# Kernel optimization log

Hardware: AMD Instinct MI355X
Metric: run time of the kernel (lower is better)

Reference implementation:

```python
import jax, jax.numpy as jnp
import numpy as np
from jax import lax

DN = ('NCHW', 'OIHW', 'NCHW')

def _conv(x, w, b, stride):
    y = lax.conv_general_dilated(x, w, (stride, stride), [(1, 1), (1, 1)], dimension_numbers=DN)
    return y + b[None, :, None, None]

def _deconv(x, w, b):
    # ConvTranspose2d(k=4, stride=2, pad=1) == conv with lhs_dilation=2, pad=k-1-p=2,
    # with w already in flipped OIHW layout.
    y = lax.conv_general_dilated(x, w, (1, 1), [(2, 2), (2, 2)], lhs_dilation=(2, 2), dimension_numbers=DN)
    return y + b[None, :, None, None]

def setup_inputs() -> dict:
    key = jax.random.key(0)
    ks = jax.random.split(key, 14)
    s = 0.05  # keep activations numerically tame
    return {
        'x':   jax.random.normal(ks[0], (16, 3, 256, 256), jnp.float32),
        'ew1': jax.random.normal(ks[1], (64, 3, 4, 4), jnp.float32) * s,
        'eb1': jax.random.normal(ks[2], (64,), jnp.float32) * s,
        'ew2': jax.random.normal(ks[3], (128, 64, 4, 4), jnp.float32) * s,
        'eb2': jax.random.normal(ks[4], (128,), jnp.float32) * s,
        'ew3': jax.random.normal(ks[5], (256, 128, 4, 4), jnp.float32) * s,
        'eb3': jax.random.normal(ks[6], (256,), jnp.float32) * s,
        'cb':  jax.random.normal(ks[7], (8192, 256), jnp.float32),
        'dw1': jax.random.normal(ks[8], (128, 256, 4, 4), jnp.float32) * s,
        'db1': jax.random.normal(ks[9], (128,), jnp.float32) * s,
        'dw2': jax.random.normal(ks[10], (64, 128, 4, 4), jnp.float32) * s,
        'db2': jax.random.normal(ks[11], (64,), jnp.float32) * s,
        'dw3': jax.random.normal(ks[12], (3, 64, 4, 4), jnp.float32) * s,
        'db3': jax.random.normal(ks[13], (3,), jnp.float32) * s,
    }

def reference(x, ew1, eb1, ew2, eb2, ew3, eb3, cb, dw1, db1, dw2, db2, dw3, db3):
    # encoder: 3 stride-2 convs with ReLU between
    h = jax.nn.relu(_conv(x, ew1, eb1, 2))
    h = jax.nn.relu(_conv(h, ew2, eb2, 2))
    feat = _conv(h, ew3, eb3, 2)                     # [B, 256, 32, 32]
    B, C, H, W = feat.shape
    flat = feat.reshape(B, C, H * W).transpose(0, 2, 1)  # [B, HW, C]
    scores = jnp.einsum('btc,kc->btk', flat, cb)     # [B, HW, K] large matrix
    indices = jnp.argmax(scores, axis=-1)            # [B, HW]
    quantized = cb[indices]                          # [B, HW, C]
    q = quantized.transpose(0, 2, 1).reshape(B, C, H, W)
    # decoder: 3 stride-2 transposed convs with ReLU between
    d = jax.nn.relu(_deconv(q, dw1, db1))
    d = jax.nn.relu(_deconv(d, dw2, db2))
    recon = _deconv(d, dw3, db3)                     # [B, 3, 256, 256]
    return recon, indices
```

## Files before the change

kernel.cpp:

```cpp
#include <hip/hip_runtime.h>
#include <hip/hip_fp16.h>
#include <cstdint>
#include <cstddef>

typedef __attribute__((ext_vector_type(8))) short short8;
typedef __attribute__((ext_vector_type(8))) _Float16 h16x8;
typedef __attribute__((ext_vector_type(4))) float f32x4;

__device__ __forceinline__ short f2bf(float x) {
  union { float f; unsigned u; } a; a.f = x;
  unsigned r = a.u + 0x7fff + ((a.u >> 16) & 1);
  return (short)(r >> 16);
}
__device__ __forceinline__ float bf2f(short s) {
  union { unsigned u; float f; } a;
  a.u = ((unsigned)(unsigned short)s) << 16; return a.f;
}
__device__ __forceinline__ void fsplit16(float v, short& h, short& l) {
  __half a = __float2half(v);
  h = (short)__half_as_ushort(a);
  l = (short)__half_as_ushort(__float2half(v - __half2float(a)));
}

__device__ __forceinline__ void ld16(const void* g, void* l) {
  __builtin_amdgcn_global_load_lds(
      (const __attribute__((address_space(1))) unsigned int*)g,
      (__attribute__((address_space(3))) unsigned int*)l, 16, 0, 0);
}

__global__ __launch_bounds__(256) void conv1_kernel(
    const float* __restrict__ x, const float* __restrict__ w,
    const float* __restrict__ bias, short* __restrict__ yh, short* __restrict__ yl)
{
  __shared__ __align__(16) float wl[64 * 48];
  __shared__ float bl[64];
  const int tid = threadIdx.x;
  for (int i = tid; i < 64 * 48; i += 256) wl[i] = w[i];
  if (tid < 64) bl[tid] = bias[tid];
  __syncthreads();
  const int n  = blockIdx.y;
  const int oh = blockIdx.x * 2 + (tid >> 7);
  const int ow = tid & 127;
  const float* xb = x + (size_t)n * 3 * 65536;
  const int ih0 = oh * 2 - 1, iw0 = ow * 2 - 1;
  float xin[48];
#pragma unroll
  for (int ic = 0; ic < 3; ++ic)
#pragma unroll
    for (int kh = 0; kh < 4; ++kh) {
      int ih = ih0 + kh;
      bool rok = (unsigned)ih < 256u;
#pragma unroll
      for (int kw = 0; kw < 4; ++kw) {
        int iw = iw0 + kw;
        xin[ic * 16 + kh * 4 + kw] =
            (rok && (unsigned)iw < 256u) ? xb[ic * 65536 + ih * 256 + iw] : 0.f;
      }
    }
  const size_t ob = ((size_t)n * 16384 + oh * 128 + ow) * 64;
  for (int g = 0; g < 8; ++g) {
    short hs[8], ls[8];
#pragma unroll
    for (int j = 0; j < 8; ++j) {
      const int oc = g * 8 + j;
      float acc = bl[oc];
      const float* wo = &wl[oc * 48];
#pragma unroll
      for (int t = 0; t < 48; ++t) acc = fmaf(wo[t], xin[t], acc);
      acc = fmaxf(acc, 0.f) * 64.f;
      fsplit16(acc, hs[j], ls[j]);
    }
    *(short8*)(yh + ob + g * 8) = *(short8*)hs;
    *(short8*)(yl + ob + g * 8) = *(short8*)ls;
  }
}

template <int COUT, int CIN>
__global__ __launch_bounds__(256) void wpack_conv(
    const float* __restrict__ w, short* __restrict__ Wh, short* __restrict__ Wl)
{
  constexpr int K = 16 * CIN;
  const int idx = blockIdx.x * 256 + threadIdx.x;
  const int oc = idx / K, k = idx - oc * K;
  const int kk = k / CIN, ic = k - kk * CIN;
  const int kh = kk >> 2, kw = kk & 3;
  float v = w[(((size_t)oc * CIN + ic) * 4 + kh) * 4 + kw] * 64.f;
  short h, l;
  fsplit16(v, h, l);
  Wh[idx] = h;
  Wl[idx] = l;
}

template <int CIN, int HIN, int COUTT, bool RELU, bool OUTF>
__global__ __launch_bounds__(256) void conv_mfma(
    const short* __restrict__ inh, const short* __restrict__ inl,
    const short* __restrict__ Wph, const short* __restrict__ Wpl,
    const float* __restrict__ bias,
    short* __restrict__ outh, short* __restrict__ outl,
    float* __restrict__ outf)
{
  constexpr int K = 16 * CIN;
  constexpr int HOUT = HIN / 2;
  constexpr int MT = 128, NPX = 128;
  constexpr int GS = (HOUT == 64) ? 6 : 5;
  constexpr int AE = 4 * MT;
  constexpr int NS = K / 32;
  constexpr float RS = 1.f / 4096.f;
  __shared__ __align__(16) short AhL[2][AE * 8];
  __shared__ __align__(16) short AlL[2][AE * 8];
  __shared__ __align__(16) float bl[MT];
  const int tid = threadIdx.x;
  const int w = tid >> 6, lane = tid & 63;
  const int wm = w >> 1, wn = w & 1;
  const int kgl = lane >> 4, cl = lane & 15;
  const int n = blockIdx.z;
  const int oc0 = blockIdx.y * MT;
  const int oh0 = blockIdx.x * (NPX / HOUT);
  if (tid < MT) bl[tid] = bias[oc0 + tid];

  f32x4 acc[4][4];
#pragma unroll
  for (int i = 0; i < 4; ++i)
#pragma unroll
    for (int j = 0; j < 4; ++j) acc[i][j] = (f32x4){0.f, 0.f, 0.f, 0.f};

  auto stageA = [&](int s, int b) {
    const int kc = s * 32;
#pragma unroll
    for (int rep = 0; rep < AE / 256; ++rep) {
      int e = rep * 256 + tid;
      int kg = e >> 7, oc_l = e & (MT - 1);
      size_t go = (size_t)(oc0 + oc_l) * K + kc + kg * 8;
      int lo = (e & ~63) * 8;
      ld16(Wph + go, &AhL[b][lo]);
      ld16(Wpl + go, &AlL[b][lo]);
    }
  };
  const h16x8 zzh = {0, 0, 0, 0, 0, 0, 0, 0};
  auto loadB = [&](int s, h16x8* bh, h16x8* blv) {
    const int kc = s * 32;
    const int kk = kc / CIN, ic0 = kc % CIN;
    const int kh = kk >> 2, kw = kk & 3;
#pragma unroll
    for (int nt = 0; nt < 4; ++nt) {
      int m = wn * 64 + nt * 16 + cl;
      int ih = 2 * (oh0 + (m >> GS)) - 1 + kh;
      int iw = 2 * (m & (HOUT - 1)) - 1 + kw;
      bool ok = ((unsigned)ih < (unsigned)HIN) && ((unsigned)iw < (unsigned)HIN);
      size_t go = ok ? ((size_t)((n * HIN + ih) * HIN + iw) * CIN + ic0 + kgl * 8)
                     : (size_t)(ic0 + kgl * 8);
      h16x8 vh = *(const h16x8*)(inh + go);
      h16x8 vl = *(const h16x8*)(inl + go);
      bh[nt] = ok ? vh : zzh;
      blv[nt] = ok ? vl : zzh;
    }
  };
  auto compute = [&](int b, const h16x8* bh, const h16x8* blv) {
    h16x8 ah[4], al[4];
#pragma unroll
    for (int mt = 0; mt < 4; ++mt) {
      int row = kgl * MT + wm * 64 + mt * 16 + cl;
      ah[mt] = *(const h16x8*)&AhL[b][row * 8];
      al[mt] = *(const h16x8*)&AlL[b][row * 8];
    }
#pragma unroll
    for (int mt = 0; mt < 4; ++mt)
#pragma unroll
      for (int nt = 0; nt < 4; ++nt) {
        acc[mt][nt] = __builtin_amdgcn_mfma_f32_16x16x32_f16(
            ah[mt], bh[nt], acc[mt][nt], 0, 0, 0);
        acc[mt][nt] = __builtin_amdgcn_mfma_f32_16x16x32_f16(
            ah[mt], blv[nt], acc[mt][nt], 0, 0, 0);
        acc[mt][nt] = __builtin_amdgcn_mfma_f32_16x16x32_f16(
            al[mt], bh[nt], acc[mt][nt], 0, 0, 0);
      }
  };

  h16x8 bhA[4], blA[4], bhB[4], blB[4];
  stageA(0, 0);
  loadB(0, bhA, blA);
  __syncthreads();
  for (int s2 = 0; s2 < NS; s2 += 2) {
    stageA(s2 + 1, 1);
    loadB(s2 + 1, bhB, blB);
    compute(0, bhA, blA);
    __syncthreads();
    if (s2 + 2 < NS) { stageA(s2 + 2, 0); loadB(s2 + 2, bhA, blA); }
    compute(1, bhB, blB);
    __syncthreads();
  }
#pragma unroll
  for (int mt = 0; mt < 4; ++mt) {
    const int oc = wm * 64 + mt * 16 + kgl * 4;
    const float4 bv = *(const float4*)&bl[oc];
#pragma unroll
    for (int nt = 0; nt < 4; ++nt) {
      const int px = wn * 64 + nt * 16 + cl;
      const int oh = oh0 + (px >> GS), ow = px & (HOUT - 1);
      const size_t ob =
          ((size_t)n * (HOUT * HOUT) + oh * HOUT + ow) * COUTT + oc0 + oc;
      float v0 = acc[mt][nt][0] * RS + bv.x;
      float v1 = acc[mt][nt][1] * RS + bv.y;
      float v2 = acc[mt][nt][2] * RS + bv.z;
      float v3 = acc[mt][nt][3] * RS + bv.w;
      if (RELU) {
        v0 = fmaxf(v0, 0.f); v1 = fmaxf(v1, 0.f);
        v2 = fmaxf(v2, 0.f); v3 = fmaxf(v3, 0.f);
      }
      if constexpr (OUTF) {
        ushort4 s;
        s.x = __half_as_ushort(__float2half(v0));
        s.y = __half_as_ushort(__float2half(v1));
        s.z = __half_as_ushort(__float2half(v2));
        s.w = __half_as_ushort(__float2half(v3));
        *(ushort4*)((unsigned short*)outh + ob) = s;
        *(float4*)(outf + ob) = make_float4(v0, v1, v2, v3);
      } else {
        short4 hh, ll;
        fsplit16(v0 * 64.f, hh.x, ll.x);
        fsplit16(v1 * 64.f, hh.y, ll.y);
        fsplit16(v2 * 64.f, hh.z, ll.z);
        fsplit16(v3 * 64.f, hh.w, ll.w);
        *(short4*)(outh + ob) = hh;
        *(short4*)(outl + ob) = ll;
      }
    }
  }
}

__global__ __launch_bounds__(256) void cb_convert(
    const float* __restrict__ cb, short* __restrict__ cbh,
    short* __restrict__ cbl, short* __restrict__ cb16)
{
  const int g = blockIdx.x * 256 + threadIdx.x;
  const float* p = cb + (size_t)g * 8;
  short hs[8], ls[8], fs[8];
#pragma unroll
  for (int u = 0; u < 8; ++u) {
    float v = p[u];
    short h = f2bf(v);
    hs[u] = h;
    ls[u] = f2bf(v - bf2f(h));
    fs[u] = (short)__half_as_ushort(__float2half(v));
  }
  *(short8*)(cbh + (size_t)g * 8) = *(short8*)hs;
  *(short8*)(cbl + (size_t)g * 8) = *(short8*)ls;
  *(short8*)(cb16 + (size_t)g * 8) = *(short8*)fs;
}

__global__ __launch_bounds__(256) void vq_mfma(
    const short* __restrict__ cb16, const short* __restrict__ ft16,
    float4* __restrict__ t4v, int4* __restrict__ t4i)
{
  __shared__ __align__(16) short Ah[2][4 * 128 * 8];
  __shared__ __align__(16) short Bh[2][4 * 128 * 8];
  const int tid = threadIdx.x;
  const int w = tid >> 6, lane = tid & 63;
  const int wm = w >> 1, wn = w & 1;
  const int tok0 = blockIdx.x * 128;
  const int split = blockIdx.y;
  const int kgl = lane >> 4, cl = lane & 15;
  const int i0 = w * 128;

  auto stage = [&](int g, int b) {
    const int tile = g >> 3, s = g & 7;
    const int code0 = split * 1024 + tile * 128;
    const int kc = s * 32;
#pragma unroll
    for (int rep = 0; rep < 2; ++rep) {
      int ib = i0 + rep * 64;
      int i = ib + lane;
      int m = i & 127, kg = i >> 7;
      size_t goffA = (size_t)(code0 + m) * 256 + kc + kg * 8;
      size_t goffB = (size_t)(tok0 + m) * 256 + kc + kg * 8;
      int loff = ib * 8;
      ld16(cb16 + goffA, &Ah[b][loff]);
      ld16(ft16 + goffB, &Bh[b][loff]);
    }
  };

  f32x4 acc[4][4];
  auto compute = [&](bool first, int b) {
    h16x8 ah[4], bh[4];
#pragma unroll
    for (int mt = 0; mt < 4; ++mt) {
      int row = wm * 64 + mt * 16 + cl;
      ah[mt] = *(const h16x8*)&Ah[b][(kgl * 128 + row) * 8];
    }
#pragma unroll
    for (int nt = 0; nt < 4; ++nt) {
      int row = wn * 64 + nt * 16 + cl;
      bh[nt] = *(const h16x8*)&Bh[b][(kgl * 128 + row) * 8];
    }
    if (first) {
#pragma unroll
      for (int mt = 0; mt < 4; ++mt)
#pragma unroll
        for (int nt = 0; nt < 4; ++nt)
          acc[mt][nt] = __builtin_amdgcn_mfma_f32_16x16x32_f16(
              ah[mt], bh[nt], (f32x4){0.f, 0.f, 0.f, 0.f}, 0, 0, 0);
    } else {
#pragma unroll
      for (int mt = 0; mt < 4; ++mt)
#pragma unroll
        for (int nt = 0; nt < 4; ++nt)
          acc[mt][nt] = __builtin_amdgcn_mfma_f32_16x16x32_f16(
              ah[mt], bh[nt], acc[mt][nt], 0, 0, 0);
    }
  };

  float sv1[4], sv2[4];
  int sj1[4], sj2[4];
#pragma unroll
  for (int nt = 0; nt < 4; ++nt) {
    sv1[nt] = -3.4e38f; sv2[nt] = -3.4e38f; sj1[nt] = 0; sj2[nt] = 0;
  }

  stage(0, 0);
  __syncthreads();
  for (int g = 0; g < 64; ++g) {
    if (g + 1 < 64) stage(g + 1, (g + 1) & 1);
    compute((g & 7) == 0, g & 1);
    if ((g & 7) == 7) {
      const int tile = g >> 3;
      const int cb2base = split * 1024 + tile * 128 + wm * 64 + kgl * 4;
#pragma unroll
      for (int nt = 0; nt < 4; ++nt)
#pragma unroll
        for (int mt = 0; mt < 4; ++mt)
#pragma unroll
          for (int r = 0; r < 4; ++r) {
            float v = acc[mt][nt][r];
            int code = cb2base + mt * 16 + r;
            bool g1 = v > sv1[nt];
            bool g2 = v > sv2[nt];
            float nv2 = g1 ? sv1[nt] : (g2 ? v : sv2[nt]);
            int nj2 = g1 ? sj1[nt] : (g2 ? code : sj2[nt]);
            sv1[nt] = g1 ? v : sv1[nt];
            sj1[nt] = g1 ? code : sj1[nt];
            sv2[nt] = nv2; sj2[nt] = nj2;
          }
    }
    __syncthreads();
  }

  float* MrgV = (float*)&Ah[0][0];
  int* MrgI = (int*)&Bh[0][0];
#pragma unroll
  for (int nt = 0; nt < 4; ++nt) {
    float mv[4] = {sv1[nt], sv2[nt], -3.4e38f, -3.4e38f};
    int mj[4] = {sj1[nt], sj2[nt], 0, 0};
#pragma unroll
    for (int st = 16; st < 64; st <<= 1) {
      float ov[4]; int oj[4];
#pragma unroll
      for (int k = 0; k < 4; ++k) {
        ov[k] = __shfl_xor(mv[k], st);
        oj[k] = __shfl_xor(mj[k], st);
      }
#pragma unroll
      for (int k = 0; k < 4; ++k) {
        if (ov[k] > mv[3]) {
          mv[3] = ov[k]; mj[3] = oj[k];
#pragma unroll
          for (int q = 3; q > 0; --q)
            if (mv[q] > mv[q - 1]) {
              float tv = mv[q]; mv[q] = mv[q - 1]; mv[q - 1] = tv;
              int tj = mj[q]; mj[q] = mj[q - 1]; mj[q - 1] = tj;
            }
        }
      }
    }
    if (lane < 16) {
      int tl = wn * 64 + nt * 16 + cl;
#pragma unroll
      for (int k = 0; k < 4; ++k) {
        MrgV[(wm * 128 + tl) * 4 + k] = mv[k];
        MrgI[(wm * 128 + tl) * 4 + k] = mj[k];
      }
    }
  }
  __syncthreads();
  if (tid < 128) {
    int tl = tid;
    float mv[4]; int mj[4];
#pragma unroll
    for (int k = 0; k < 4; ++k) { mv[k] = MrgV[tl * 4 + k]; mj[k] = MrgI[tl * 4 + k]; }
#pragma unroll
    for (int k = 0; k < 4; ++k) {
      float ov = MrgV[(128 + tl) * 4 + k];
      int oj = MrgI[(128 + tl) * 4 + k];
      if (ov > mv[3]) {
        mv[3] = ov; mj[3] = oj;
#pragma unroll
        for (int q = 3; q > 0; --q)
          if (mv[q] > mv[q - 1]) {
            float tv = mv[q]; mv[q] = mv[q - 1]; mv[q - 1] = tv;
            int tj = mj[q]; mj[q] = mj[q - 1]; mj[q - 1] = tj;
          }
      }
    }
    size_t o = (size_t)split * 16384 + tok0 + tl;
    t4v[o] = make_float4(mv[0], mv[1], mv[2], mv[3]);
    t4i[o] = make_int4(mj[0], mj[1], mj[2], mj[3]);
  }
}

__global__ __launch_bounds__(256) void vq_rescore(
    const float4* __restrict__ t4v, const int4* __restrict__ t4i,
    const float* __restrict__ featc, const float* __restrict__ cb,
    int* __restrict__ fidx, float* __restrict__ idx_out)
{
  const int t = blockIdx.x * 256 + threadIdx.x;
  float vs[4] = {-3.4e38f, -3.4e38f, -3.4e38f, -3.4e38f};
  int is[4] = {0, 0, 0, 0};
#pragma unroll
  for (int sp = 0; sp < 8; ++sp) {
    float4 v4 = t4v[(size_t)sp * 16384 + t];
    int4 i4 = t4i[(size_t)sp * 16384 + t];
    float vv[4] = {v4.x, v4.y, v4.z, v4.w};
    int ii[4] = {i4.x, i4.y, i4.z, i4.w};
#pragma unroll
    for (int k = 0; k < 4; ++k) {
      if (vv[k] > vs[3]) {
        vs[3] = vv[k]; is[3] = ii[k];
#pragma unroll
        for (int q = 3; q > 0; --q)
          if (vs[q] > vs[q - 1]) {
            float tv = vs[q]; vs[q] = vs[q - 1]; vs[q - 1] = tv;
            int ti = is[q]; is[q] = is[q - 1]; is[q - 1] = ti;
          }
      }
    }
  }
  const float4* fc = (const float4*)(featc + (size_t)t * 256);
  const float4* c0 = (const float4*)(cb + (size_t)is[0] * 256);
  const float4* c1 = (const float4*)(cb + (size_t)is[1] * 256);
  const float4* c2 = (const float4*)(cb + (size_t)is[2] * 256);
  const float4* c3 = (const float4*)(cb + (size_t)is[3] * 256);
  float s0 = 0.f, s1 = 0.f, s2 = 0.f, s3 = 0.f;
  for (int k4 = 0; k4 < 64; ++k4) {
    float4 f = fc[k4];
    float4 w0 = c0[k4], w1 = c1[k4], w2 = c2[k4], w3 = c3[k4];
    s0 = fmaf(w0.x, f.x, fmaf(w0.y, f.y, fmaf(w0.z, f.z, fmaf(w0.w, f.w, s0))));
    s1 = fmaf(w1.x, f.x, fmaf(w1.y, f.y, fmaf(w1.z, f.z, fmaf(w1.w, f.w, s1))));
    s2 = fmaf(w2.x, f.x, fmaf(w2.y, f.y, fmaf(w2.z, f.z, fmaf(w2.w, f.w, s2))));
    s3 = fmaf(w3.x, f.x, fmaf(w3.y, f.y, fmaf(w3.z, f.z, fmaf(w3.w, f.w, s3))));
  }
  float best = s0; int bi = is[0];
  float sv[3] = {s1, s2, s3};
  int si2[3] = {is[1], is[2], is[3]};
#pragma unroll
  for (int c = 0; c < 3; ++c)
    if (sv[c] > best || (sv[c] == best && si2[c] < bi)) { best = sv[c]; bi = si2[c]; }
  fidx[t] = bi;
  idx_out[t] = (float)bi;
}

template <int COUT, int CIN>
__global__ __launch_bounds__(256) void wpack(
    const float* __restrict__ w, short* __restrict__ Ah, short* __restrict__ Al)
{
  constexpr int K = 4 * CIN;
  const int idx = blockIdx.x * 256 + threadIdx.x;
  const int par = idx / (COUT * K);
  const int rem = idx % (COUT * K);
  const int oc = rem / K;
  const int k = rem % K;
  const int kk = k / CIN, ic = k % CIN;
  const int kh = 2 * (kk >> 1) + (par >> 1);
  const int kw = 2 * (kk & 1) + (par & 1);
  float v = w[(((size_t)oc * CIN + ic) * 4 + kh) * 4 + kw];
  short h = f2bf(v);
  Ah[idx] = h;
  Al[idx] = f2bf(v - bf2f(h));
}

__global__ __launch_bounds__(256) void gather2(
    const short* __restrict__ cbh, const short* __restrict__ cbl,
    const int* __restrict__ fidx, short* __restrict__ qTh, short* __restrict__ qTl)
{
  const int tid = threadIdx.x;
  const int gt = blockIdx.x * 64 + (tid >> 2);
  const int part = tid & 3;
  const int code = fidx[gt];
  const short8* sh = (const short8*)(cbh + (size_t)code * 256 + part * 64);
  const short8* sl = (const short8*)(cbl + (size_t)code * 256 + part * 64);
  short8* dh = (short8*)(qTh + (size_t)gt * 256 + part * 64);
  short8* dl = (short8*)(qTl + (size_t)gt * 256 + part * 64);
#pragma unroll
  for (int j = 0; j < 8; ++j) { dh[j] = sh[j]; dl[j] = sl[j]; }
}

template <int CIN, int GRID, int COUT, int NPX, int WM, int WN, bool OUT_HALF>
__global__ __launch_bounds__(256) void deconv_mfma(
    const short* __restrict__ inh, const short* __restrict__ inl,
    const short* __restrict__ Aph, const short* __restrict__ Apl,
    const float* __restrict__ bias, void* __restrict__ out_h,
    void* __restrict__ out_l)
{
  constexpr int K = 4 * CIN, HOUT = 2 * GRID, AE = 4 * COUT;
  constexpr int GS = (GRID == 32) ? 5 : 6;
  constexpr int NS = K / 32;
  __shared__ __align__(16) short AhL[2][AE * 8];
  __shared__ __align__(16) short AlL[2][AE * 8];
  __shared__ float bl[COUT];
  const int tid = threadIdx.x;
  const int w = tid >> 6, lane = tid & 63;
  const int wm = w / WN, wn = w % WN;
  const int kgl = lane >> 4, cl = lane & 15;
  const int par = blockIdx.y, n = blockIdx.z;
  const int pr = par >> 1, pc = par & 1;
  const int Ut0 = blockIdx.x * (NPX / GRID);
  if (tid < COUT) bl[tid] = bias[tid];

  f32x4 acc[4][4];
#pragma unroll
  for (int i = 0; i < 4; ++i)
#pragma unroll
    for (int j = 0; j < 4; ++j) acc[i][j] = (f32x4){0.f, 0.f, 0.f, 0.f};

  auto stageA = [&](int s, int b) {
    const int kc = s * 32;
#pragma unroll
    for (int rep = 0; rep < AE / 256; ++rep) {
      int e = rep * 256 + tid;
      int kg = e / COUT, oc_l = e % COUT;
      size_t go = ((size_t)(par * COUT + oc_l)) * K + kc + kg * 8;
      int lo = (e & ~63) * 8;
      ld16(Aph + go, &AhL[b][lo]);
      ld16(Apl + go, &AlL[b][lo]);
    }
  };
  const short8 zz = {0, 0, 0, 0, 0, 0, 0, 0};
  auto loadB = [&](int s, short8* bh, short8* blo) {
    const int kc = s * 32;
    const int kk = kc / CIN, ic0 = kc % CIN;
    const int dr = (kk >> 1) + pr - 1, dc = (kk & 1) + pc - 1;
#pragma unroll
    for (int nt = 0; nt < 4; ++nt) {
      int m = wn * 64 + nt * 16 + cl;
      int sU = Ut0 + (m >> GS) + dr;
      int sV = (m & (GRID - 1)) + dc;
      bool ok = (unsigned)sU < (unsigned)GRID && (unsigned)sV < (unsigned)GRID;
      long pix = (long)(n * GRID + sU) * GRID + sV;
      size_t go = ok ? (size_t)(pix * CIN + ic0 + kgl * 8)
                     : (size_t)(ic0 + kgl * 8);
      short8 vh = *(const short8*)(inh + go);
      short8 vl = *(const short8*)(inl + go);
      bh[nt] = ok ? vh : zz;
      blo[nt] = ok ? vl : zz;
    }
  };
  auto compute = [&](int b, const short8* bh, const short8* blo) {
    short8 ah[4], al[4];
#pragma unroll
    for (int mt = 0; mt < 4; ++mt) {
      int row = kgl * COUT + wm * 64 + mt * 16 + cl;
      ah[mt] = *(const short8*)&AhL[b][row * 8];
      al[mt] = *(const short8*)&AlL[b][row * 8];
    }
#pragma unroll
    for (int mt = 0; mt < 4; ++mt)
#pragma unroll
      for (int nt = 0; nt < 4; ++nt) {
        acc[mt][nt] = __builtin_amdgcn_mfma_f32_16x16x32_bf16(
            ah[mt], bh[nt], acc[mt][nt], 0, 0, 0);
        acc[mt][nt] = __builtin_amdgcn_mfma_f32_16x16x32_bf16(
            ah[mt], blo[nt], acc[mt][nt], 0, 0, 0);
        acc[mt][nt] = __builtin_amdgcn_mfma_f32_16x16x32_bf16(
            al[mt], bh[nt], acc[mt][nt], 0, 0, 0);
      }
  };

  short8 bhA[4], blA[4], bhB[4], blB[4];
  stageA(0, 0);
  loadB(0, bhA, blA);
  __syncthreads();
  for (int s2 = 0; s2 < NS; s2 += 2) {
    stageA(s2 + 1, 1);
    loadB(s2 + 1, bhB, blB);
    compute(0, bhA, blA);
    __syncthreads();
    if (s2 + 2 < NS) { stageA(s2 + 2, 0); loadB(s2 + 2, bhA, blA); }
    compute(1, bhB, blB);
    __syncthreads();
  }
#pragma unroll
  for (int mt = 0; mt < 4; ++mt) {
    const int oc = wm * 64 + mt * 16 + kgl * 4;
    const float4 bv = *(const float4*)&bl[oc];
#pragma unroll
    for (int nt = 0; nt < 4; ++nt) {
      const int px = wn * 64 + nt * 16 + cl;
      const int U = Ut0 + (px >> GS), V = px & (GRID - 1);
      const int r = 2 * U + pr, c = 2 * V + pc;
      const size_t ob = ((size_t)n * HOUT * HOUT + (size_t)r * HOUT + c) * COUT + oc;
      float v0 = fmaxf(acc[mt][nt][0] + bv.x, 0.f);
      float v1 = fmaxf(acc[mt][nt][1] + bv.y, 0.f);
      float v2 = fmaxf(acc[mt][nt][2] + bv.z, 0.f);
      float v3 = fmaxf(acc[mt][nt][3] + bv.w, 0.f);
      if constexpr (OUT_HALF) {
        ushort4 s;
        s.x = __half_as_ushort(__float2half(v0));
        s.y = __half_as_ushort(__float2half(v1));
        s.z = __half_as_ushort(__float2half(v2));
        s.w = __half_as_ushort(__float2half(v3));
        *(ushort4*)((unsigned short*)out_h + ob) = s;
      } else {
        short4 hh, ll;
        hh.x = f2bf(v0); ll.x = f2bf(v0 - bf2f(hh.x));
        hh.y = f2bf(v1); ll.y = f2bf(v1 - bf2f(hh.y));
        hh.z = f2bf(v2); ll.z = f2bf(v2 - bf2f(hh.z));
        hh.w = f2bf(v3); ll.w = f2bf(v3 - bf2f(hh.w));
        *(short4*)((short*)out_h + ob) = hh;
        *(short4*)((short*)out_l + ob) = ll;
      }
    }
  }
}

__global__ __launch_bounds__(256) void deconv3_kernel(
    const __half* __restrict__ d2, const float* __restrict__ w,
    const float* __restrict__ bias, float* __restrict__ y)
{
  __shared__ __align__(16) float Xl[108 * 68];
  __shared__ __align__(16) float wl[4 * 4 * 3 * 64];
  const int tid = threadIdx.x;
  for (int i = tid; i < 3072; i += 256) {
    int oc = i >> 10, ic = (i >> 4) & 63, kh = (i >> 2) & 3, kw = i & 3;
    int par = (kh & 1) * 2 + (kw & 1), kidx = (kh >> 1) * 2 + (kw >> 1);
    wl[((par * 4 + kidx) * 3 + oc) * 64 + ic] = w[i];
  }
  const int n = blockIdx.z, r0 = blockIdx.y * 8, c0 = blockIdx.x * 32;
  const int gr0 = (r0 >> 1) - 1, gc0 = (c0 >> 1) - 1;
  for (int e = tid; e < 1728; e += 256) {
    int pl = e >> 4, sub = e & 15;
    int rr = pl / 18, cc = pl - rr * 18;
    int gr = gr0 + rr, gc = gc0 + cc;
    float4 v = make_float4(0.f, 0.f, 0.f, 0.f);
    if ((unsigned)gr < 128u && (unsigned)gc < 128u) {
      const __half2* p =
          (const __half2*)(d2 + ((size_t)(n * 16384 + gr * 128 + gc) * 64 + sub * 4));
      float2 f0 = __half22float2(p[0]);
      float2 f1 = __half22float2(p[1]);
      v = make_float4(f0.x, f0.y, f1.x, f1.y);
    }
    *(float4*)&Xl[pl * 68 + sub * 4] = v;
  }
  __syncthreads();
  const int wv = tid >> 6, lane = tid & 63;
  const int pr = wv >> 1, pc = wv & 1;
  const int Ul = lane >> 4, Vl = lane & 15;
  float a0 = bias[0], a1 = bias[1], a2 = bias[2];
  const int parb = wv * 768;
#pragma unroll
  for (int ic4 = 0; ic4 < 16; ++ic4) {
    float4 xv[4];
#pragma unroll
    for (int t = 0; t < 4; ++t) {
      int lr = Ul + (t >> 1) + pr, lc = Vl + (t & 1) + pc;
      xv[t] = *(const float4*)&Xl[(lr * 18 + lc) * 68 + ic4 * 4];
    }
#pragma unroll
    for (int t = 0; t < 4; ++t) {
      float4 w0 = *(const float4*)&wl[parb + (t * 3 + 0) * 64 + ic4 * 4];
      float4 w1 = *(const float4*)&wl[parb + (t * 3 + 1) * 64 + ic4 * 4];
      float4 w2 = *(const float4*)&wl[parb + (t * 3 + 2) * 64 + ic4 * 4];
      a0 = fmaf(w0.x, xv[t].x, fmaf(w0.y, xv[t].y, fmaf(w0.z, xv[t].z, fmaf(w0.w, xv[t].w, a0))));
      a1 = fmaf(w1.x, xv[t].x, fmaf(w1.y, xv[t].y, fmaf(w1.z, xv[t].z, fmaf(w1.w, xv[t].w, a1))));
      a2 = fmaf(w2.x, xv[t].x, fmaf(w2.y, xv[t].y, fmaf(w2.z, xv[t].z, fmaf(w2.w, xv[t].w, a2))));
    }
  }
  const int r = r0 + 2 * Ul + pr, c = c0 + 2 * Vl + pc;
  float* yn = y + (size_t)n * 3 * 65536 + r * 256 + c;
  yn[0] = a0;
  yn[65536] = a1;
  yn[131072] = a2;
}

extern "C" void kernel_launch(void* const* d_in, const int* in_sizes, int n_in,
                              void* d_out, int out_size, void* d_ws, size_t ws_size,
                              hipStream_t stream)
{
  const float* x   = (const float*)d_in[0];
  const float* ew1 = (const float*)d_in[1];
  const float* eb1 = (const float*)d_in[2];
  const float* ew2 = (const float*)d_in[3];
  const float* eb2 = (const float*)d_in[4];
  const float* ew3 = (const float*)d_in[5];
  const float* eb3 = (const float*)d_in[6];
  const float* cb  = (const float*)d_in[7];
  const float* dw1 = (const float*)d_in[8];
  const float* db1 = (const float*)d_in[9];
  const float* dw2 = (const float*)d_in[10];
  const float* db2 = (const float*)d_in[11];
  const float* dw3 = (const float*)d_in[12];
  const float* db3 = (const float*)d_in[13];

  float* recon = (float*)d_out;
  float* idxf  = (float*)d_out + 3145728;

  const size_t MB = 1048576ull;
  char* ws = (char*)d_ws;
  short* h1h = (short*)ws;
  short* h1l = (short*)(ws + 32 * MB);
  short* h2h = (short*)(ws + 64 * MB);
  short* h2l = (short*)(ws + 80 * MB);
  short* ft16  = (short*)ws;
  float* featf = (float*)(ws + 16 * MB);
  short* cbh  = (short*)(ws + 64 * MB);
  short* cbl  = (short*)(ws + 68 * MB);
  short* cb16 = (short*)(ws + 72 * MB);
  float4* t4v = (float4*)(ws + 80 * MB);
  int4*   t4i = (int4*)(ws + 82 * MB);
  int*    fidx = (int*)(ws + 92 * MB);
  short* A1h = (short*)(ws + 76 * MB);
  short* A1l = (short*)(ws + 77 * MB);
  short* A2h = (short*)(ws + 78 * MB);
  short* A2l = (short*)(ws + 78 * MB + 262144);
  short* qTh = (short*)ws;
  short* qTl = (short*)(ws + 8 * MB);
  short* d1h = (short*)(ws + 32 * MB);
  short* d1l = (short*)(ws + 48 * MB);
  __half* d2 = (__half*)ws;
  short* W2h = (short*)recon;
  short* W2l = W2h + 131072;
  short* W3h = W2h + 262144;
  short* W3l = W2h + 786432;

  conv1_kernel<<<dim3(64, 16), 256, 0, stream>>>(x, ew1, eb1, h1h, h1l);
  wpack_conv<128, 64><<<dim3(512), 256, 0, stream>>>(ew2, W2h, W2l);
  conv_mfma<64, 128, 128, true, false><<<dim3(32, 1, 16), 256, 0, stream>>>(
      h1h, h1l, W2h, W2l, eb2, h2h, h2l, nullptr);
  wpack_conv<256, 128><<<dim3(2048), 256, 0, stream>>>(ew3, W3h, W3l);
  conv_mfma<128, 64, 256, false, true><<<dim3(8, 2, 16), 256, 0, stream>>>(
      h2h, h2l, W3h, W3l, eb3, ft16, nullptr, featf);

  cb_convert<<<dim3(1024), 256, 0, stream>>>(cb, cbh, cbl, cb16);
  vq_mfma<<<dim3(128, 8), 256, 0, stream>>>(cb16, ft16, t4v, t4i);
  vq_rescore<<<dim3(64), 256, 0, stream>>>(t4v, t4i, featf, cb, fidx, idxf);

  wpack<128, 256><<<dim3(2048), 256, 0, stream>>>(dw1, A1h, A1l);
  wpack<64, 128><<<dim3(512), 256, 0, stream>>>(dw2, A2h, A2l);
  gather2<<<dim3(256), 256, 0, stream>>>(cbh, cbl, fidx, qTh, qTl);

  deconv_mfma<256, 32, 128, 128, 2, 2, false>
      <<<dim3(8, 4, 16), 256, 0, stream>>>(qTh, qTl, A1h, A1l, db1, d1h, d1l);
  deconv_mfma<128, 64, 64, 256, 1, 4, true>
      <<<dim3(16, 4, 16), 256, 0, stream>>>(d1h, d1l, A2h, A2l, db2, d2, d2);
  deconv3_kernel<<<dim3(8, 32, 16), 256, 0, stream>>>(d2, dw3, db3, recon);
}
```

Before: 916.4 us.

## Load VQ score operands directly from global and pack code index into float

The VQ scoring kernel stops staging codebook and feature tiles through double-buffered LDS with per-step barriers. Each wave now reads its MFMA fragments directly from global memory (relying on cache), and occupancy is hinted at 3 blocks per CU. The candidate code index is packed into the low 11 mantissa bits of each score, so the top-2 tracking becomes plain fmin/fmax and the separate index arrays, shuffles and stores go away. The cost is perturbed score values, which rescoring is meant to absorb, and possibly less efficient uncoalesced global loads in place of LDS reuse.

```diff
diff --git a/kernel.cpp b/kernel.cpp
--- a/kernel.cpp
+++ b/kernel.cpp
@@ -248,125 +248,88 @@
   *(short8*)(cb16 + (size_t)g * 8) = *(short8*)fs;
 }
 
-__global__ __launch_bounds__(256) void vq_mfma(
+__global__ __launch_bounds__(256, 3) void vq_mfma(
     const short* __restrict__ cb16, const short* __restrict__ ft16,
-    float4* __restrict__ t4v, int4* __restrict__ t4i)
-{
-  __shared__ __align__(16) short Ah[2][4 * 128 * 8];
-  __shared__ __align__(16) short Bh[2][4 * 128 * 8];
+    float4* __restrict__ t4v)
+{
+  __shared__ __align__(16) float MrgV[256 * 4];
   const int tid = threadIdx.x;
   const int w = tid >> 6, lane = tid & 63;
   const int wm = w >> 1, wn = w & 1;
   const int tok0 = blockIdx.x * 128;
   const int split = blockIdx.y;
   const int kgl = lane >> 4, cl = lane & 15;
-  const int i0 = w * 128;
-
-  auto stage = [&](int g, int b) {
-    const int tile = g >> 3, s = g & 7;
-    const int code0 = split * 1024 + tile * 128;
-    const int kc = s * 32;
-#pragma unroll
-    for (int rep = 0; rep < 2; ++rep) {
-      int ib = i0 + rep * 64;
-      int i = ib + lane;
-      int m = i & 127, kg = i >> 7;
-      size_t goffA = (size_t)(code0 + m) * 256 + kc + kg * 8;
-      size_t goffB = (size_t)(tok0 + m) * 256 + kc + kg * 8;
-      int loff = ib * 8;
-      ld16(cb16 + goffA, &Ah[b][loff]);
-      ld16(ft16 + goffB, &Bh[b][loff]);
-    }
-  };
-
-  f32x4 acc[4][4];
-  auto compute = [&](bool first, int b) {
-    h16x8 ah[4], bh[4];
-#pragma unroll
-    for (int mt = 0; mt < 4; ++mt) {
-      int row = wm * 64 + mt * 16 + cl;
-      ah[mt] = *(const h16x8*)&Ah[b][(kgl * 128 + row) * 8];
-    }
-#pragma unroll
-    for (int nt = 0; nt < 4; ++nt) {
-      int row = wn * 64 + nt * 16 + cl;
-      bh[nt] = *(const h16x8*)&Bh[b][(kgl * 128 + row) * 8];
-    }
-    if (first) {
+
+  const short* pA[4];
+  const short* pB[4];
+#pragma unroll
+  for (int mt = 0; mt < 4; ++mt)
+    pA[mt] = cb16 + ((size_t)(split * 1024 + wm * 64 + mt * 16 + cl)) * 256 + kgl * 8;
+#pragma unroll
+  for (int nt = 0; nt < 4; ++nt)
+    pB[nt] = ft16 + ((size_t)(tok0 + wn * 64 + nt * 16 + cl)) * 256 + kgl * 8;
+
+  float m1[4], m2[4];
+#pragma unroll
+  for (int nt = 0; nt < 4; ++nt) { m1[nt] = -3.4e38f; m2[nt] = -3.4e38f; }
+  const unsigned orbase0 = (unsigned)(wm * 64 + kgl * 4);
+
+  for (int tile = 0; tile < 8; ++tile) {
+    f32x4 acc[4][4];
+    f32x4 z4 = (f32x4){0.f, 0.f, 0.f, 0.f};
+#pragma unroll
+    for (int s = 0; s < 8; ++s) {
+      h16x8 af[4], bf[4];
+#pragma unroll
+      for (int mt = 0; mt < 4; ++mt) af[mt] = *(const h16x8*)(pA[mt] + s * 32);
+#pragma unroll
+      for (int nt = 0; nt < 4; ++nt) bf[nt] = *(const h16x8*)(pB[nt] + s * 32);
 #pragma unroll
       for (int mt = 0; mt < 4; ++mt)
 #pragma unroll
-        for (int nt = 0; nt < 4; ++nt)
-          acc[mt][nt] = __builtin_amdgcn_mfma_f32_16x16x32_f16(
-              ah[mt], bh[nt], (f32x4){0.f, 0.f, 0.f, 0.f}, 0, 0, 0);
-    } else {
+        for (int nt = 0; nt < 4; ++nt) {
+          if (s == 0)
+            acc[mt][nt] = __builtin_amdgcn_mfma_f32_16x16x32_f16(
+                af[mt], bf[nt], z4, 0, 0, 0);
+          else
+            acc[mt][nt] = __builtin_amdgcn_mfma_f32_16x16x32_f16(
+                af[mt], bf[nt], acc[mt][nt], 0, 0, 0);
+        }
+    }
+    const unsigned orb = (unsigned)(tile * 128) + orbase0;
+#pragma unroll
+    for (int nt = 0; nt < 4; ++nt)
 #pragma unroll
       for (int mt = 0; mt < 4; ++mt)
 #pragma unroll
-        for (int nt = 0; nt < 4; ++nt)
-          acc[mt][nt] = __builtin_amdgcn_mfma_f32_16x16x32_f16(
-              ah[mt], bh[nt], acc[mt][nt], 0, 0, 0);
-    }
-  };
-
-  float sv1[4], sv2[4];
-  int sj1[4], sj2[4];
+        for (int r = 0; r < 4; ++r) {
+          union { float f; unsigned u; } pv;
+          pv.f = acc[mt][nt][r];
+          pv.u = (pv.u & 0xFFFFF800u) | (orb + (unsigned)(mt * 16 + r));
+          float t = fminf(m1[nt], pv.f);
+          m1[nt] = fmaxf(m1[nt], pv.f);
+          m2[nt] = fmaxf(m2[nt], t);
+        }
+#pragma unroll
+    for (int mt = 0; mt < 4; ++mt) pA[mt] += 128 * 256;
+  }
+
 #pragma unroll
   for (int nt = 0; nt < 4; ++nt) {
-    sv1[nt] = -3.4e38f; sv2[nt] = -3.4e38f; sj1[nt] = 0; sj2[nt] = 0;
-  }
-
-  stage(0, 0);
-  __syncthreads();
-  for (int g = 0; g < 64; ++g) {
-    if (g + 1 < 64) stage(g + 1, (g + 1) & 1);
-    compute((g & 7) == 0, g & 1);
-    if ((g & 7) == 7) {
-      const int tile = g >> 3;
-      const int cb2base = split * 1024 + tile * 128 + wm * 64 + kgl * 4;
-#pragma unroll
-      for (int nt = 0; nt < 4; ++nt)
-#pragma unroll
-        for (int mt = 0; mt < 4; ++mt)
-#pragma unroll
-          for (int r = 0; r < 4; ++r) {
-            float v = acc[mt][nt][r];
-            int code = cb2base + mt * 16 + r;
-            bool g1 = v > sv1[nt];
-            bool g2 = v > sv2[nt];
-            float nv2 = g1 ? sv1[nt] : (g2 ? v : sv2[nt]);
-            int nj2 = g1 ? sj1[nt] : (g2 ? code : sj2[nt]);
-            sv1[nt] = g1 ? v : sv1[nt];
-            sj1[nt] = g1 ? code : sj1[nt];
-            sv2[nt] = nv2; sj2[nt] = nj2;
-          }
-    }
-    __syncthreads();
-  }
-
-  float* MrgV = (float*)&Ah[0][0];
-  int* MrgI = (int*)&Bh[0][0];
-#pragma unroll
-  for (int nt = 0; nt < 4; ++nt) {
-    float mv[4] = {sv1[nt], sv2[nt], -3.4e38f, -3.4e38f};
-    int mj[4] = {sj1[nt], sj2[nt], 0, 0};
+    float mv[4] = {m1[nt], m2[nt], -3.4e38f, -3.4e38f};
 #pragma unroll
     for (int st = 16; st < 64; st <<= 1) {
-      float ov[4]; int oj[4];
-#pragma unroll
-      for (int k = 0; k < 4; ++k) {
-        ov[k] = __shfl_xor(mv[k], st);
-        oj[k] = __shfl_xor(mj[k], st);
-      }
+      float ov[4];
+#pragma unroll
+      for (int k = 0; k < 4; ++k) ov[k] = __shfl_xor(mv[k], st);
 #pragma unroll
       for (int k = 0; k < 4; ++k) {
         if (ov[k] > mv[3]) {
-          mv[3] = ov[k]; mj[3] = oj[k];
+          mv[3] = ov[k];
 #pragma unroll
           for (int q = 3; q > 0; --q)
             if (mv[q] > mv[q - 1]) {
               float tv = mv[q]; mv[q] = mv[q - 1]; mv[q - 1] = tv;
-              int tj = mj[q]; mj[q] = mj[q - 1]; mj[q - 1] = tj;
             }
         }
       }
@@ -374,42 +337,36 @@
     if (lane < 16) {
       int tl = wn * 64 + nt * 16 + cl;
 #pragma unroll
-      for (int k = 0; k < 4; ++k) {
-        MrgV[(wm * 128 + tl) * 4 + k] = mv[k];
-        MrgI[(wm * 128 + tl) * 4 + k] = mj[k];
-      }
+      for (int k = 0; k < 4; ++k) MrgV[(wm * 128 + tl) * 4 + k] = mv[k];
     }
   }
   __syncthreads();
   if (tid < 128) {
     int tl = tid;
-    float mv[4]; int mj[4];
-#pragma unroll
-    for (int k = 0; k < 4; ++k) { mv[k] = MrgV[tl * 4 + k]; mj[k] = MrgI[tl * 4 + k]; }
+    float mv[4];
+#pragma unroll
+    for (int k = 0; k < 4; ++k) mv[k] = MrgV[tl * 4 + k];
 #pragma unroll
     for (int k = 0; k < 4; ++k) {
       float ov = MrgV[(128 + tl) * 4 + k];
-      int oj = MrgI[(128 + tl) * 4 + k];
       if (ov > mv[3]) {
-        mv[3] = ov; mj[3] = oj;
+        mv[3] = ov;
 #pragma unroll
         for (int q = 3; q > 0; --q)
           if (mv[q] > mv[q - 1]) {
             float tv = mv[q]; mv[q] = mv[q - 1]; mv[q - 1] = tv;
-            int tj = mj[q]; mj[q] = mj[q - 1]; mj[q - 1] = tj;
           }
       }
     }
     size_t o = (size_t)split * 16384 + tok0 + tl;
     t4v[o] = make_float4(mv[0], mv[1], mv[2], mv[3]);
-    t4i[o] = make_int4(mj[0], mj[1], mj[2], mj[3]);
   }
 }
 
 __global__ __launch_bounds__(256) void vq_rescore(
-    const float4* __restrict__ t4v, const int4* __restrict__ t4i,
-    const float* __restrict__ featc, const float* __restrict__ cb,
-    int* __restrict__ fidx, float* __restrict__ idx_out)
+    const float4* __restrict__ t4v, const float* __restrict__ featc,
+    const float* __restrict__ cb, int* __restrict__ fidx,
+    float* __restrict__ idx_out)
 {
   const int t = blockIdx.x * 256 + threadIdx.x;
   float vs[4] = {-3.4e38f, -3.4e38f, -3.4e38f, -3.4e38f};
@@ -417,13 +374,14 @@
 #pragma unroll
   for (int sp = 0; sp < 8; ++sp) {
     float4 v4 = t4v[(size_t)sp * 16384 + t];
-    int4 i4 = t4i[(size_t)sp * 16384 + t];
     float vv[4] = {v4.x, v4.y, v4.z, v4.w};
-    int ii[4] = {i4.x, i4.y, i4.z, i4.w};
 #pragma unroll
     for (int k = 0; k < 4; ++k) {
-      if (vv[k] > vs[3]) {
-        vs[3] = vv[k]; is[3] = ii[k];
+      float v = vv[k];
+      union { float f; unsigned u; } pu; pu.f = v;
+      int ii = sp * 1024 + (int)(pu.u & 0x7FFu);
+      if (v > vs[3]) {
+        vs[3] = v; is[3] = ii;
 #pragma unroll
         for (int q = 3; q > 0; --q)
           if (vs[q] > vs[q - 1]) {
@@ -713,7 +671,6 @@
   short* cbl  = (short*)(ws + 68 * MB);
   short* cb16 = (short*)(ws + 72 * MB);
   float4* t4v = (float4*)(ws + 80 * MB);
-  int4*   t4i = (int4*)(ws + 82 * MB);
   int*    fidx = (int*)(ws + 92 * MB);
   short* A1h = (short*)(ws + 76 * MB);
   short* A1l = (short*)(ws + 77 * MB);
@@ -738,8 +695,8 @@
       h2h, h2l, W3h, W3l, eb3, ft16, nullptr, featf);
 
   cb_convert<<<dim3(1024), 256, 0, stream>>>(cb, cbh, cbl, cb16);
-  vq_mfma<<<dim3(128, 8), 256, 0, stream>>>(cb16, ft16, t4v, t4i);
-  vq_rescore<<<dim3(64), 256, 0, stream>>>(t4v, t4i, featf, cb, fidx, idxf);
+  vq_mfma<<<dim3(128, 8), 256, 0, stream>>>(cb16, ft16, t4v);
+  vq_rescore<<<dim3(64), 256, 0, stream>>>(t4v, featf, cb, fidx, idxf);
 
   wpack<128, 256><<<dim3(2048), 256, 0, stream>>>(dw1, A1h, A1l);
   wpack<64, 128><<<dim3(512), 256, 0, stream>>>(dw2, A2h, A2l);
```

New measurement: 1.049 ms. +14.4%, slower.
